# Kernel tuning notes

Hardware: AMD Instinct MI355X
Metric: run time of the kernel (lower is better)

The kernel has to match this reference:

```python
import jax, jax.numpy as jnp
import numpy as np

N_CLUSTERS = 8
N_DIMS = 4
N_POINTS = 2_000_000


def setup_inputs() -> dict:
    key = jax.random.key(0)
    k1, k2, k3, k4 = jax.random.split(key, 4)
    return {
        "X": jax.random.normal(k1, (N_POINTS, N_DIMS), dtype=jnp.float32),
        "means": jax.random.normal(k2, (N_CLUSTERS, N_DIMS), dtype=jnp.float32),
        "chols": jax.random.normal(k3, (N_CLUSTERS, N_DIMS, N_DIMS), dtype=jnp.float32),
        "weights": jax.random.normal(k4, (N_CLUSTERS,), dtype=jnp.float32),
        "it": 0,
    }


def reference(X, means, chols, weights, it):
    N, D = X.shape
    K = means.shape[0]
    # sigmas[k] = tril(L_k) @ tril(L_k)^T + I  (cholesky_comp)
    L = jnp.tril(chols)                                   # [K,D,D]
    sigmas = L @ jnp.swapaxes(L, -1, -2) + jnp.eye(D, dtype=X.dtype)
    S_inv = jnp.linalg.inv(sigmas)                        # [K,D,D]
    dets = jnp.linalg.det(sigmas)                         # [K]
    two_pi_D = (2.0 * jnp.pi) ** D
    # per-cluster Gaussian densities over all points: dens[k,n]
    diff = X[None, :, :] - means[:, None, :]              # [K,N,D]
    mahal = jnp.einsum('knd,kde,kne->kn', diff, S_inv, diff)  # [K,N]
    dens = jnp.exp(-0.5 * mahal) / jnp.sqrt(two_pi_D * dets)[:, None]
    # pairwise softmax weights over all K^2 (i,j) products w_i*w_j
    wij = weights[:, None] * weights[None, :]             # [K,K]
    W = jax.nn.softmax(wij.reshape(-1)).reshape(K, K)
    # squared-mixture normaliser: z = sum_ij W_ij * N(mu_i; mu_j, S_i+S_j)
    Ssum = sigmas[:, None] + sigmas[None, :]              # [K,K,D,D]
    det_sum = jnp.linalg.det(Ssum)                        # [K,K]
    mdiff = means[:, None, :] - means[None, :, :]         # [K,K,D]
    md = jnp.einsum('ijd,ijde,ije->ij', mdiff, jnp.linalg.inv(Ssum), mdiff)
    norm_term = jnp.exp(-0.5 * md) / jnp.sqrt(two_pi_D * det_sum)
    z = jnp.sum(W * norm_term)
    # numerator: sum_ij W_ij dens_i dens_j  (factored to avoid [K^2,N])
    num = jnp.einsum('in,jn,ij->n', dens, dens, W)        # [N]
    pdf = num / z
    # forward: -(logsumexp over points of log pdf) / N
    out = -(jax.scipy.special.logsumexp(jnp.log(pdf)) / N)
    return out
```

## Files before the change

kernel.cpp:

```cpp
#include <hip/hip_runtime.h>
#include <math.h>


struct WsLayout {
  double P[36][32];
  double Wp[36];
  double logz;
  float a2[8][10];
  float bb[8][4];
  float cc[8];
};

__device__ inline void chol4(const double S[4][4], double G[4][4]) {
  #pragma unroll
  for (int i = 0; i < 4; ++i) {
    #pragma unroll
    for (int j = 0; j < 4; ++j) {
      if (j > i) { G[i][j] = 0.0; continue; }
      double s = S[i][j];
      #pragma unroll
      for (int m = 0; m < 4; ++m) if (m < j) s -= G[i][m] * G[j][m];
      if (i == j) G[i][j] = sqrt(s);
      else        G[i][j] = s / G[j][j];
    }
  }
}

__global__ void prep_kernel(const float* __restrict__ means,
                            const float* __restrict__ chols,
                            const float* __restrict__ weights,
                            WsLayout* ws) {
  __shared__ double sig[8][4][4];
  const double LOG2E = 1.4426950408889634074;
  const double LN2PI = 1.8378770664093454836;
  const int t = threadIdx.x;

  if (t < 8) {
    const int k = t;
    double L[4][4], S[4][4];
    #pragma unroll
    for (int i = 0; i < 4; ++i)
      #pragma unroll
      for (int j = 0; j < 4; ++j)
        L[i][j] = (j <= i) ? (double)chols[k * 16 + i * 4 + j] : 0.0;
    #pragma unroll
    for (int i = 0; i < 4; ++i)
      #pragma unroll
      for (int j = 0; j < 4; ++j) {
        double s = (i == j) ? 1.0 : 0.0;
        #pragma unroll
        for (int m = 0; m < 4; ++m) s += L[i][m] * L[j][m];
        S[i][j] = s;
        sig[k][i][j] = s;
      }
    double G[4][4];
    chol4(S, G);
    const double logdet =
        2.0 * (log(G[0][0]) + log(G[1][1]) + log(G[2][2]) + log(G[3][3]));
    double Gi[4][4];
    #pragma unroll
    for (int j = 0; j < 4; ++j) {
      #pragma unroll
      for (int i = 0; i < 4; ++i) {
        if (i < j) { Gi[i][j] = 0.0; continue; }
        double s = (i == j) ? 1.0 : 0.0;
        #pragma unroll
        for (int m = 0; m < 4; ++m)
          if (m >= j && m < i) s -= G[i][m] * Gi[m][j];
        Gi[i][j] = s / G[i][i];
      }
    }
    double A[4][4];
    #pragma unroll
    for (int i = 0; i < 4; ++i)
      #pragma unroll
      for (int j = 0; j < 4; ++j) {
        double s = 0.0;
        #pragma unroll
        for (int m = 0; m < 4; ++m) s += Gi[m][i] * Gi[m][j];
        A[i][j] = s;
      }
    double mu[4];
    #pragma unroll
    for (int i = 0; i < 4; ++i) mu[i] = (double)means[k * 4 + i];
    double bmu[4];
    #pragma unroll
    for (int i = 0; i < 4; ++i) {
      double s = 0.0;
      #pragma unroll
      for (int j = 0; j < 4; ++j) s += A[i][j] * mu[j];
      bmu[i] = s;
    }
    double muAmu = 0.0;
    #pragma unroll
    for (int i = 0; i < 4; ++i) muAmu += mu[i] * bmu[i];
    const double logcoef = -0.5 * (4.0 * LN2PI + logdet);
    int tt = 0;
    #pragma unroll
    for (int i = 0; i < 4; ++i)
      #pragma unroll
      for (int j = i; j < 4; ++j, ++tt)
        ws->a2[k][tt] =
            (float)(-0.5 * LOG2E * A[i][j] * ((i == j) ? 1.0 : 2.0));
    #pragma unroll
    for (int i = 0; i < 4; ++i) ws->bb[k][i] = (float)(LOG2E * bmu[i]);
    ws->cc[k] = (float)(LOG2E * (logcoef - 0.5 * muAmu));
  }
  __syncthreads();

  const int i = t >> 3, j = t & 7;
  const double wij = (double)weights[i] * (double)weights[j];
  double m = wij;
  #pragma unroll
  for (int o = 32; o > 0; o >>= 1) {
    double x = __shfl_xor(m, o, 64);
    m = fmax(m, x);
  }
  const double e = exp(wij - m);
  double ssum = e;
  #pragma unroll
  for (int o = 32; o > 0; o >>= 1) ssum += __shfl_xor(ssum, o, 64);
  const double Wij = e / ssum;

  double SS[4][4];
  #pragma unroll
  for (int a = 0; a < 4; ++a)
    #pragma unroll
    for (int b = 0; b < 4; ++b) SS[a][b] = sig[i][a][b] + sig[j][a][b];
  double G2[4][4];
  chol4(SS, G2);
  const double logdetS =
      2.0 * (log(G2[0][0]) + log(G2[1][1]) + log(G2[2][2]) + log(G2[3][3]));
  double bvec[4], y[4];
  #pragma unroll
  for (int a = 0; a < 4; ++a)
    bvec[a] = (double)means[i * 4 + a] - (double)means[j * 4 + a];
  #pragma unroll
  for (int a = 0; a < 4; ++a) {
    double s = bvec[a];
    #pragma unroll
    for (int mm = 0; mm < 4; ++mm) if (mm < a) s -= G2[a][mm] * y[mm];
    y[a] = s / G2[a][a];
  }
  const double md = y[0]*y[0] + y[1]*y[1] + y[2]*y[2] + y[3]*y[3];
  double zterm = Wij * exp(-0.5 * md - 0.5 * (4.0 * LN2PI + logdetS));
  #pragma unroll
  for (int o = 32; o > 0; o >>= 1) zterm += __shfl_xor(zterm, o, 64);
  if (t == 0) ws->logz = log(zterm);

  if (i <= j) {
    const int u = 8 * i - (i * (i - 1)) / 2 + (j - i);
    ws->Wp[u] = Wij * ((i == j) ? 1.0 : 2.0);
  }
  double* Pf = &ws->P[0][0];
  for (int u = t; u < 36 * 32; u += 64) Pf[u] = 0.0;
}

__global__ __launch_bounds__(256, 4) void point_kernel(
    const float4* __restrict__ X, const float* __restrict__ par,
    double* __restrict__ accg, int n) {
  float a2[8][10], bb[8][4], cc[8];
  #pragma unroll
  for (int k = 0; k < 8; ++k) {
    #pragma unroll
    for (int u = 0; u < 10; ++u) a2[k][u] = par[k * 10 + u];
    #pragma unroll
    for (int u = 0; u < 4; ++u) bb[k][u] = par[80 + k * 4 + u];
    cc[k] = par[112 + k];
  }
  float acc[36];
  #pragma unroll
  for (int u = 0; u < 36; ++u) acc[u] = 0.0f;

  const int S = gridDim.x * blockDim.x;
  const int idx = blockIdx.x * blockDim.x + threadIdx.x;
  for (int base = idx; base < n; base += 4 * S) {
    float4 v[4];
    float kill[4];
    #pragma unroll
    for (int j = 0; j < 4; ++j) {
      const int ij = base + j * S;
      const bool ok = ij < n;
      kill[j] = ok ? 0.0f : -1.0e30f;
      v[j] = X[ok ? ij : 0];
    }
    #pragma unroll
    for (int j = 0; j < 4; ++j) {
      const float4 vv = v[j];
      const float p[10] = {vv.x * vv.x, vv.x * vv.y, vv.x * vv.z, vv.x * vv.w,
                           vv.y * vv.y, vv.y * vv.z, vv.y * vv.w,
                           vv.z * vv.z, vv.z * vv.w, vv.w * vv.w};
      float d[8];
      #pragma unroll
      for (int k = 0; k < 8; ++k) {
        float a = cc[k] + kill[j];
        #pragma unroll
        for (int u = 0; u < 10; ++u) a = fmaf(a2[k][u], p[u], a);
        a = fmaf(bb[k][0], vv.x, a);
        a = fmaf(bb[k][1], vv.y, a);
        a = fmaf(bb[k][2], vv.z, a);
        a = fmaf(bb[k][3], vv.w, a);
        d[k] = __builtin_amdgcn_exp2f(a);
      }
      int u = 0;
      #pragma unroll
      for (int a_ = 0; a_ < 8; ++a_)
        #pragma unroll
        for (int b_ = a_; b_ < 8; ++b_, ++u)
          acc[u] = fmaf(d[a_], d[b_], acc[u]);
    }
  }

  const int lane = threadIdx.x & 63;
  const int wid = threadIdx.x >> 6;
  __shared__ float lred[4][36];
  #pragma unroll
  for (int u = 0; u < 36; ++u) {
    float vv = acc[u];
    #pragma unroll
    for (int o = 32; o > 0; o >>= 1) vv += __shfl_xor(vv, o, 64);
    if (lane == 0) lred[wid][u] = vv;
  }
  __syncthreads();
  if (threadIdx.x < 36) {
    const double s = (double)lred[0][threadIdx.x] + (double)lred[1][threadIdx.x] +
                     (double)lred[2][threadIdx.x] + (double)lred[3][threadIdx.x];
    unsafeAtomicAdd(&accg[threadIdx.x * 32 + (blockIdx.x & 31)], s);
  }
}

__global__ void final_kernel(const WsLayout* __restrict__ ws,
                             float* __restrict__ out, int n) {
  const int t = threadIdx.x;
  double val = 0.0;
  if (t < 36) {
    double s = 0.0;
    #pragma unroll
    for (int b = 0; b < 32; ++b) s += ws->P[t][b];
    val = ws->Wp[t] * s;
  }
  #pragma unroll
  for (int o = 32; o > 0; o >>= 1) val += __shfl_xor(val, o, 64);
  if (t == 0) out[0] = (float)(-(log(val) - ws->logz) / (double)n);
}

extern "C" void kernel_launch(void* const* d_in, const int* in_sizes, int n_in,
                              void* d_out, int out_size, void* d_ws, size_t ws_size,
                              hipStream_t stream) {
  const float* X       = (const float*)d_in[0];
  const float* means   = (const float*)d_in[1];
  const float* chols   = (const float*)d_in[2];
  const float* weights = (const float*)d_in[3];
  const int npoints = in_sizes[0] / 4;

  WsLayout* ws = (WsLayout*)d_ws;
  prep_kernel<<<1, 64, 0, stream>>>(means, chols, weights, ws);
  point_kernel<<<2048, 256, 0, stream>>>((const float4*)X, &ws->a2[0][0],
                                         &ws->P[0][0], npoints);
  final_kernel<<<1, 64, 0, stream>>>(ws, (float*)d_out, npoints);
}
```

Baseline: 112.2 us.

## Fuse final reduction into point kernel via last-block counter and widen per-thread batch

New measurement: 138.5 us. 23.5% more time.

```diff
diff --git a/kernel.cpp b/kernel.cpp
--- a/kernel.cpp
+++ b/kernel.cpp
@@ -2,10 +2,14 @@
 #include <math.h>
 
 
+#define NSLOT 64
+
 struct WsLayout {
-  double P[36][32];
+  double P[36 * NSLOT];
   double Wp[36];
   double logz;
+  unsigned int ctr;
+  unsigned int pad_;
   float a2[8][10];
   float bb[8][4];
   float cc[8];
@@ -146,19 +150,20 @@
   double zterm = Wij * exp(-0.5 * md - 0.5 * (4.0 * LN2PI + logdetS));
   #pragma unroll
   for (int o = 32; o > 0; o >>= 1) zterm += __shfl_xor(zterm, o, 64);
-  if (t == 0) ws->logz = log(zterm);
+  if (t == 0) { ws->logz = log(zterm); ws->ctr = 0u; }
 
   if (i <= j) {
     const int u = 8 * i - (i * (i - 1)) / 2 + (j - i);
     ws->Wp[u] = Wij * ((i == j) ? 1.0 : 2.0);
   }
-  double* Pf = &ws->P[0][0];
-  for (int u = t; u < 36 * 32; u += 64) Pf[u] = 0.0;
-}
-
-__global__ __launch_bounds__(256, 4) void point_kernel(
-    const float4* __restrict__ X, const float* __restrict__ par,
-    double* __restrict__ accg, int n) {
+  for (int u = t; u < 36 * NSLOT; u += 64) ws->P[u] = 0.0;
+}
+
+__global__ __launch_bounds__(256, 2) void point_kernel(
+    const float4* __restrict__ X, const WsLayout* __restrict__ wsc,
+    double* __restrict__ P, unsigned int* ctr, float* __restrict__ out,
+    int n) {
+  const float* par = &wsc->a2[0][0];
   float a2[8][10], bb[8][4], cc[8];
   #pragma unroll
   for (int k = 0; k < 8; ++k) {
@@ -174,74 +179,84 @@
 
   const int S = gridDim.x * blockDim.x;
   const int idx = blockIdx.x * blockDim.x + threadIdx.x;
-  for (int base = idx; base < n; base += 4 * S) {
-    float4 v[4];
-    float kill[4];
-    #pragma unroll
-    for (int j = 0; j < 4; ++j) {
-      const int ij = base + j * S;
-      const bool ok = ij < n;
-      kill[j] = ok ? 0.0f : -1.0e30f;
-      v[j] = X[ok ? ij : 0];
-    }
-    #pragma unroll
-    for (int j = 0; j < 4; ++j) {
-      const float4 vv = v[j];
-      const float p[10] = {vv.x * vv.x, vv.x * vv.y, vv.x * vv.z, vv.x * vv.w,
-                           vv.y * vv.y, vv.y * vv.z, vv.y * vv.w,
-                           vv.z * vv.z, vv.z * vv.w, vv.w * vv.w};
-      float d[8];
-      #pragma unroll
-      for (int k = 0; k < 8; ++k) {
-        float a = cc[k] + kill[j];
-        #pragma unroll
-        for (int u = 0; u < 10; ++u) a = fmaf(a2[k][u], p[u], a);
-        a = fmaf(bb[k][0], vv.x, a);
-        a = fmaf(bb[k][1], vv.y, a);
-        a = fmaf(bb[k][2], vv.z, a);
-        a = fmaf(bb[k][3], vv.w, a);
-        d[k] = __builtin_amdgcn_exp2f(a);
-      }
-      int u = 0;
-      #pragma unroll
-      for (int a_ = 0; a_ < 8; ++a_)
-        #pragma unroll
-        for (int b_ = a_; b_ < 8; ++b_, ++u)
-          acc[u] = fmaf(d[a_], d[b_], acc[u]);
-    }
+  float4 v[8];
+  float kill[8];
+  #pragma unroll
+  for (int j = 0; j < 8; ++j) {
+    const int ij = idx + j * S;
+    const bool ok = ij < n;
+    kill[j] = ok ? 0.0f : -1.0e30f;
+    v[j] = X[ok ? ij : 0];
+  }
+  #pragma unroll
+  for (int j = 0; j < 8; ++j) {
+    const float4 vv = v[j];
+    const float p[10] = {vv.x * vv.x, vv.x * vv.y, vv.x * vv.z, vv.x * vv.w,
+                         vv.y * vv.y, vv.y * vv.z, vv.y * vv.w,
+                         vv.z * vv.z, vv.z * vv.w, vv.w * vv.w};
+    float d[8];
+    #pragma unroll
+    for (int k = 0; k < 8; ++k) {
+      float a = cc[k] + kill[j];
+      #pragma unroll
+      for (int u = 0; u < 10; ++u) a = fmaf(a2[k][u], p[u], a);
+      a = fmaf(bb[k][0], vv.x, a);
+      a = fmaf(bb[k][1], vv.y, a);
+      a = fmaf(bb[k][2], vv.z, a);
+      a = fmaf(bb[k][3], vv.w, a);
+      d[k] = __builtin_amdgcn_exp2f(a);
+    }
+    int u = 0;
+    #pragma unroll
+    for (int a_ = 0; a_ < 8; ++a_)
+      #pragma unroll
+      for (int b_ = a_; b_ < 8; ++b_, ++u)
+        acc[u] = fmaf(d[a_], d[b_], acc[u]);
   }
 
   const int lane = threadIdx.x & 63;
   const int wid = threadIdx.x >> 6;
-  __shared__ float lred[4][36];
+  __shared__ double lred[4][36];
   #pragma unroll
   for (int u = 0; u < 36; ++u) {
     float vv = acc[u];
     #pragma unroll
     for (int o = 32; o > 0; o >>= 1) vv += __shfl_xor(vv, o, 64);
-    if (lane == 0) lred[wid][u] = vv;
+    if (lane == 0) lred[wid][u] = (double)vv;
   }
   __syncthreads();
   if (threadIdx.x < 36) {
-    const double s = (double)lred[0][threadIdx.x] + (double)lred[1][threadIdx.x] +
-                     (double)lred[2][threadIdx.x] + (double)lred[3][threadIdx.x];
-    unsafeAtomicAdd(&accg[threadIdx.x * 32 + (blockIdx.x & 31)], s);
-  }
-}
-
-__global__ void final_kernel(const WsLayout* __restrict__ ws,
-                             float* __restrict__ out, int n) {
-  const int t = threadIdx.x;
-  double val = 0.0;
-  if (t < 36) {
-    double s = 0.0;
-    #pragma unroll
-    for (int b = 0; b < 32; ++b) s += ws->P[t][b];
-    val = ws->Wp[t] * s;
-  }
-  #pragma unroll
-  for (int o = 32; o > 0; o >>= 1) val += __shfl_xor(val, o, 64);
-  if (t == 0) out[0] = (float)(-(log(val) - ws->logz) / (double)n);
+    const double s = lred[0][threadIdx.x] + lred[1][threadIdx.x] +
+                     lred[2][threadIdx.x] + lred[3][threadIdx.x];
+    unsafeAtomicAdd(&P[threadIdx.x * NSLOT + (blockIdx.x & (NSLOT - 1))], s);
+  }
+  __syncthreads();
+
+  __shared__ int amLast;
+  if (threadIdx.x == 0) {
+    __threadfence();
+    const unsigned int old = atomicAdd(ctr, 1u);
+    amLast = (old == gridDim.x - 1u);
+    __threadfence();
+  }
+  __syncthreads();
+  if (amLast) {
+    double val = 0.0;
+    for (int i = (int)threadIdx.x; i < 36 * NSLOT; i += 256) {
+      const int u = i >> 6;
+      const double pv = unsafeAtomicAdd(&P[i], 0.0);
+      val += wsc->Wp[u] * pv;
+    }
+    #pragma unroll
+    for (int o = 32; o > 0; o >>= 1) val += __shfl_xor(val, o, 64);
+    __shared__ double fin[4];
+    if (lane == 0) fin[wid] = val;
+    __syncthreads();
+    if (threadIdx.x == 0) {
+      const double tot = fin[0] + fin[1] + fin[2] + fin[3];
+      out[0] = (float)(-(log(tot) - wsc->logz) / (double)n);
+    }
+  }
 }
 
 extern "C" void kernel_launch(void* const* d_in, const int* in_sizes, int n_in,
@@ -255,7 +270,6 @@
 
   WsLayout* ws = (WsLayout*)d_ws;
   prep_kernel<<<1, 64, 0, stream>>>(means, chols, weights, ws);
-  point_kernel<<<2048, 256, 0, stream>>>((const float4*)X, &ws->a2[0][0],
-                                         &ws->P[0][0], npoints);
-  final_kernel<<<1, 64, 0, stream>>>(ws, (float*)d_out, npoints);
-}
+  point_kernel<<<1024, 256, 0, stream>>>((const float4*)X, ws, ws->P, &ws->ctr,
+                                         (float*)d_out, npoints);
+}
```
